# Kernel tuning notes

Hardware: AMD Instinct MI355X
Metric: run time of the kernel (lower is better)

The kernel has to match this reference:

```python
import jax, jax.numpy as jnp
import numpy as np

D_MODEL = 1024
NHEAD = 16
HEAD_DIM = D_MODEL // NHEAD
SCALE = 1.0 / np.sqrt(HEAD_DIM).astype(np.float32)
B, L = 2, 2048
NEG_INF = -1e30


def setup_inputs() -> dict:
    key = jax.random.key(0)
    ks = jax.random.split(key, 12)
    xav = np.sqrt(6.0 / (D_MODEL + D_MODEL)).astype(np.float32)  # xavier_uniform gain=1
    def lin_w(k):
        return jax.random.uniform(k, (D_MODEL, D_MODEL), jnp.float32, -xav, xav)
    x = jax.random.normal(ks[0], (B, L, D_MODEL), jnp.float32)
    role_mask = jax.random.randint(ks[1], (B, L), 0, 2, jnp.int32)
    # causal attention mask: True = masked (upper triangle above diagonal)
    attn_mask = jnp.triu(jnp.ones((L, L), jnp.bool_), k=1)
    # random key padding: True = padded key
    key_padding_mask = jax.random.randint(ks[2], (B, L), 0, 2, jnp.int32).astype(jnp.bool_)
    return {
        "x": x,
        "role_mask": role_mask,
        "attn_mask": attn_mask,
        "key_padding_mask": key_padding_mask,
        "Wq": lin_w(ks[3]), "bq": jnp.zeros((D_MODEL,), jnp.float32),
        "Wk": lin_w(ks[4]), "bk": jnp.zeros((D_MODEL,), jnp.float32),
        "Wv": lin_w(ks[5]), "bv": jnp.zeros((D_MODEL,), jnp.float32),
        "Wo": lin_w(ks[6]), "bo": jnp.zeros((D_MODEL,), jnp.float32),
        "delta": jnp.asarray(1.0, jnp.float32),
    }


def reference(x, role_mask, attn_mask, key_padding_mask,
              Wq, bq, Wk, bk, Wv, bv, Wo, bo, delta):
    Bb, Ll, Dd = x.shape
    def heads(t):  # [B,L,D] -> [B,H,L,hd]
        return t.reshape(Bb, Ll, NHEAD, HEAD_DIM).transpose(0, 2, 1, 3)
    Q = heads(x @ Wq.T + bq)
    K = heads(x @ Wk.T + bk)
    V = heads(x @ Wv.T + bv)
    scores = jnp.einsum('bhqd,bhkd->bhqk', Q, K) * SCALE  # [B,H,L,L]
    same_role = (role_mask[:, :, None] == role_mask[:, None, :])  # [B,L,L]
    scores = scores + (same_role.astype(scores.dtype) * delta)[:, None, :, :]
    scores = jnp.where(attn_mask[None, None, :, :], -jnp.inf, scores)
    scores = jnp.where(key_padding_mask[:, None, None, :], -jnp.inf, scores)
    attn = jax.nn.softmax(scores, axis=-1)
    attn = jnp.nan_to_num(attn, nan=0.0, posinf=0.0, neginf=0.0)
    out = jnp.einsum('bhqk,bhkd->bhqd', attn, V)
    out = out.transpose(0, 2, 1, 3).reshape(Bb, Ll, Dd)
    return out @ Wo.T + bo
```

## Files before the change

### kernel.cpp

```cpp
#include <hip/hip_runtime.h>
#include <hip/hip_bf16.h>

#define DM 1024
#define NH 16
#define HD 64
#define BB 2
#define LL 2048
#define SCALE 0.125f
#define NEG_BIG -1e30f
#define LOG2E 1.4426950408889634f
#define SC2 (SCALE * LOG2E)
#define FIXM 16.0f
#define SLOTB 8448
#define POOL0_SLOTS 960

typedef __bf16 bf16;
typedef __bf16 bf16x8 __attribute__((ext_vector_type(8)));
typedef __bf16 bf16x4 __attribute__((ext_vector_type(4)));
typedef float f32x4 __attribute__((ext_vector_type(4)));

static __device__ inline bf16x8 load8(const bf16* p) {
    return *reinterpret_cast<const bf16x8*>(p);
}

static __device__ inline float scrub(float x) {
    union { float f; unsigned u; } c; c.f = x;
    return ((c.u & 0x7F800000u) == 0x7F800000u) ? 0.f : x;
}

typedef __attribute__((address_space(1))) const unsigned char ga_t;
typedef __attribute__((address_space(3))) unsigned char ls_t;
static __device__ inline void gload_lds16(const void* g, void* l) {
    __builtin_amdgcn_global_load_lds((ga_t*)g, (ls_t*)l, 16, 0, 0);
}

__global__ __launch_bounds__(256) void prep_all(
    const float* __restrict__ x,
    const float* __restrict__ Wq, const float* __restrict__ Wk,
    const float* __restrict__ Wv, const float* __restrict__ Wo,
    bf16* __restrict__ xb, bf16* __restrict__ Wqb, bf16* __restrict__ Wkb,
    bf16* __restrict__ Wvb, bf16* __restrict__ Wob,
    const int* __restrict__ role, const void* __restrict__ kpad,
    const float* __restrict__ deltap, float2* __restrict__ biasG)
{
    const int tid = threadIdx.x;
    const int gid = blockIdx.x;
    if (gid < 2048) {
        const float* src; bf16* dst; size_t base;
        if (gid < 1024) { src = x; dst = xb; base = (size_t)gid * 1024; }
        else {
            const int wsel = (gid - 1024) >> 8;
            src = (wsel == 0) ? Wq : (wsel == 1) ? Wk : (wsel == 2) ? Wv : Wo;
            dst = (wsel == 0) ? Wqb : (wsel == 1) ? Wkb : (wsel == 2) ? Wvb : Wob;
            base = (size_t)((gid - 1024) & 255) * 1024;
        }
#pragma unroll
        for (int it = 0; it < 4; it++) {
            const size_t i = base + it * 256 + tid;
            const f32x4 v = ((const f32x4*)src)[i];
            bf16x4 o;
            o[0] = (bf16)v[0]; o[1] = (bf16)v[1]; o[2] = (bf16)v[2]; o[3] = (bf16)v[3];
            ((bf16x4*)dst)[i] = o;
        }
        return;
    }
    const unsigned char* kb = (const unsigned char*)kpad;
    int f3F = 0, fLow = 0, fOff = 0;
    for (int i = (tid & 63); i < BB * LL; i += 64) {
        const unsigned char v = kb[i];
        if (v == 0x3F) f3F = 1;
        if ((i & 3) < 2 && v) fLow = 1;
        if ((i & 3) && v) fOff = 1;
    }
    const int mode = __any(f3F) ? (__any(fLow) ? 3 : 2) : (__any(fOff) ? 1 : 0);
    const float d2 = scrub(deltap[0]) * LOG2E;
    const int idx = (gid - 2048) * 256 + tid;
    const bool pad = (mode == 0) ? (((const int*)kpad)[idx] != 0)
                   : (mode == 1) ? (((const unsigned char*)kpad)[idx] != 0)
                   : (mode == 2) ? (((const float*)kpad)[idx] != 0.f)
                                 : (((const unsigned short*)kpad)[idx] != 0);
    const int r = role[idx];
    const float base = (pad ? NEG_BIG : 0.f) - FIXM;
    float2 o;
    o.x = base + ((r == 0) ? d2 : 0.f);
    o.y = base + ((r == 1) ? d2 : 0.f);
    biasG[idx] = o;
}

__global__ __launch_bounds__(256) void qkv_bf16(
    const bf16* __restrict__ xb,
    const bf16* __restrict__ Wqb, const bf16* __restrict__ Wkb, const bf16* __restrict__ Wvb,
    const float* __restrict__ bq, const float* __restrict__ bk, const float* __restrict__ bv,
    bf16* __restrict__ qw, bf16* __restrict__ kw, bf16* __restrict__ vw)
{
    __shared__ bf16 As[128 * 32];
    __shared__ bf16 Bs[128 * 32];
    const int tid = threadIdx.x;
    const int lane = tid & 63, w = tid >> 6;
    const int wm = w >> 1, wn = w & 1;
    const int ln = lane & 15, quad = lane >> 4;

    const int lin = blockIdx.y * 32 + blockIdx.x;
    const int xcd = lin & 7;
    const int t = lin >> 3;
    const int mloc = t & 3;
    const int yy = t >> 2;
    const int m0 = (xcd * 4 + mloc) * 128;
    const int sel = yy >> 3;
    const int nloc0 = (yy & 7) * 128;

    const bf16* Wb = (sel == 0) ? Wqb : ((sel == 1) ? Wkb : Wvb);
    const float* bias = (sel == 0) ? bq : ((sel == 1) ? bk : bv);
    bf16* dstw = (sel == 0) ? qw : ((sel == 1) ? kw : vw);

    const int rA = lane >> 2;
    const int cA = (lane & 3) * 8;

    f32x4 acc[4][4] = {};
    for (int k0 = 0; k0 < DM; k0 += 32) {
        __syncthreads();
#pragma unroll
        for (int s = 0; s < 2; s++) {
            const int r0 = s * 64 + w * 16;
            gload_lds16(xb + (size_t)(m0 + r0 + rA) * DM + k0 + cA, &As[r0 * 32]);
            gload_lds16(Wb + (size_t)(nloc0 + r0 + rA) * DM + k0 + cA, &Bs[r0 * 32]);
        }
        __syncthreads();
        bf16x8 a[4], b[4];
#pragma unroll
        for (int mi = 0; mi < 4; mi++)
            a[mi] = *(bf16x8*)&As[(wm * 64 + mi * 16 + ln) * 32 + quad * 8];
#pragma unroll
        for (int ni = 0; ni < 4; ni++)
            b[ni] = *(bf16x8*)&Bs[(wn * 64 + ni * 16 + ln) * 32 + quad * 8];
#pragma unroll
        for (int mi = 0; mi < 4; mi++)
#pragma unroll
            for (int ni = 0; ni < 4; ni++)
                acc[mi][ni] = __builtin_amdgcn_mfma_f32_16x16x32_bf16(a[mi], b[ni], acc[mi][ni], 0, 0, 0);
    }

#pragma unroll
    for (int mi = 0; mi < 4; mi++) {
#pragma unroll
        for (int ni = 0; ni < 4; ni++) {
            const int ncol = nloc0 + wn * 64 + ni * 16 + ln;
            const float bv_ = bias[ncol];
            const int hh = ncol >> 6, dd = ncol & 63;
#pragma unroll
            for (int i = 0; i < 4; i++) {
                const int row = m0 + wm * 64 + mi * 16 + quad * 4 + i;
                const int bb = row >> 11, llr = row & (LL - 1);
                const bf16 v = (bf16)scrub(acc[mi][ni][i] + bv_);
                dstw[(((size_t)(bb * NH + hh) * LL) + llr) * HD + dd] = v;
            }
        }
    }
}

__global__ __launch_bounds__(256) void vtrans(
    const bf16* __restrict__ vw, bf16* __restrict__ vtw)
{
    __shared__ bf16 T[64][72];
    const int l0 = blockIdx.x * 64;
    const int bh = blockIdx.y;
    const int tid = threadIdx.x;
#pragma unroll
    for (int it = 0; it < 2; it++) {
        const int idx = it * 256 + tid;
        const int row = idx >> 3, c8 = (idx & 7) * 8;
        *(bf16x8*)&T[row][c8] = load8(vw + ((size_t)bh * LL + l0 + row) * HD + c8);
    }
    __syncthreads();
#pragma unroll
    for (int it = 0; it < 2; it++) {
        const int idx = it * 256 + tid;
        const int dd = idx >> 3, pg = (idx & 7) * 8;
        bf16x8 o;
#pragma unroll
        for (int j = 0; j < 8; j++) {
            const int p = pg + j;
            const int kl = (p & 3) * 16 + (p >> 2);
            o[j] = T[kl][dd];
        }
        *(bf16x8*)(vtw + ((size_t)bh * HD + dd) * LL + l0 + pg) = o;
    }
}

#define PSTR 32
__global__ __launch_bounds__(256) void attn_v12(
    const bf16* __restrict__ qw, const bf16* __restrict__ kw, const bf16* __restrict__ vtw,
    const int* __restrict__ role, const float2* __restrict__ biasG,
    char* __restrict__ pool0, char* __restrict__ pool1,
    bf16* __restrict__ attn_out)
{
    const int lin = blockIdx.y * 60 + blockIdx.x;
    const int xcd = lin & 7;
    const int t = lin >> 3;
    const int xg = t % 60;
    const int g = t / 60;
    const int bh = g * 8 + xcd;

    int qb, c;
    if (xg < 24)      { qb = 31 - xg / 3; c = xg % 3; }
    else if (xg < 48) { qb = 23 - (xg - 24) / 2; c = (xg - 24) % 2; }
    else              { qb = 59 - xg; c = 0; }
    const int nch = (qb + 12) / 12;

    __shared__ bf16 Ks[2][2][64 * 32];
    __shared__ bf16 Vs[2][2][64 * 32];
    __shared__ bf16 Ps[4][2][16 * PSTR];

    const int tid = threadIdx.x;
    const int lane = tid & 63, w = tid >> 6;
    const int col = lane & 15, quad = lane >> 4;
    const int h = bh & (NH - 1), b = bh >> 4;
    const int q0 = qb * 64 + w * 16;

    const bf16* qbase = qw + (size_t)((b * NH + h) * LL) * HD;
    const bf16* kbase = kw + (size_t)((b * NH + h) * LL) * HD;
    const bf16* vbase = vtw + (size_t)((b * NH + h) * HD) * LL;
    const float2* bias2 = biasG + (size_t)b * LL;
    const int* rrow = role + b * LL;

    const int srow = lane >> 2;
    const int swz = ((lane & 3) ^ ((lane >> 3) & 3)) * 8;
    const bf16* ksrc = kbase + (size_t)(w * 16 + srow) * HD + swz;
    const bf16* vsrc = vbase + (size_t)(w * 16 + srow) * LL + swz;

    bf16x8 qf[2];
    qf[0] = load8(qbase + (size_t)(q0 + col) * HD + quad * 8);
    qf[1] = load8(qbase + (size_t)(q0 + col) * HD + 32 + quad * 8);

    bf16x8 ones;
#pragma unroll
    for (int j = 0; j < 8; j++) ones[j] = (bf16)1.0f;

    int role_q[4];
#pragma unroll
    for (int i = 0; i < 4; i++) role_q[i] = rrow[q0 + quad * 4 + i];

    f32x4 ol = {};
    f32x4 o[4] = {};

    const int t0 = c * 12;
    const int t1 = (t0 + 12 < qb + 1) ? t0 + 12 : qb + 1;

    {
        const int kp = t0 * 64;
#pragma unroll
        for (int st = 0; st < 2; st++)
            gload_lds16(ksrc + (size_t)kp * HD + st * 32, &Ks[0][st][w * 512]);
#pragma unroll
        for (int kh = 0; kh < 2; kh++)
            gload_lds16(vsrc + kp + kh * 32, &Vs[0][kh][w * 512]);
    }

    const int rs = (quad ^ ((col >> 1) & 3)) * 8;

    for (int kt = t0; kt < t1; kt++) {
        const int cur = (kt - t0) & 1;
        __syncthreads();

        if (kt + 1 < t1) {
            const int k1 = (kt + 1) * 64;
#pragma unroll
            for (int st = 0; st < 2; st++)
                gload_lds16(ksrc + (size_t)k1 * HD + st * 32, &Ks[cur ^ 1][st][w * 512]);
#pragma unroll
            for (int kh = 0; kh < 2; kh++)
                gload_lds16(vsrc + k1 + kh * 32, &Vs[cur ^ 1][kh][w * 512]);
        }

        const int k0 = kt * 64;
        float2 bb[4];
#pragma unroll
        for (int ns = 0; ns < 4; ns++) bb[ns] = bias2[k0 + ns * 16 + col];

        f32x4 s[4] = {};
#pragma unroll
        for (int st = 0; st < 2; st++) {
#pragma unroll
            for (int ns = 0; ns < 4; ns++) {
                const bf16x8 kf = *(bf16x8*)&Ks[cur][st][(ns * 16 + col) * 32 + rs];
                s[ns] = __builtin_amdgcn_mfma_f32_16x16x32_bf16(qf[st], kf, s[ns], 0, 0, 0);
            }
        }
        const bool diag = (kt == qb);
        const int half = col >> 3;
#pragma unroll
        for (int i = 0; i < 4; i++) {
            bf16x4 pk;
#pragma unroll
            for (int ns = 0; ns < 4; ns++) {
                float sv = fmaf(s[ns][i], SC2, role_q[i] ? bb[ns].y : bb[ns].x);
                if (diag && (k0 + ns * 16 + col) > q0 + quad * 4 + i) sv = NEG_BIG;
                pk[ns] = (bf16)exp2f(sv);
            }
            const int row = quad * 4 + i;
            const int sw = (quad * 2 + (i >> 1)) & 3;
            const int ew = ((((col & 7) >> 1) ^ sw) * 8) + (col & 1) * 4;
            *(bf16x4*)&Ps[w][half][row * PSTR + ew] = pk;
        }
        bf16x8 pf[2];
#pragma unroll
        for (int st = 0; st < 2; st++)
            pf[st] = *(bf16x8*)&Ps[w][st][col * PSTR + rs];
#pragma unroll
        for (int ns = 0; ns < 4; ns++) {
#pragma unroll
            for (int kh = 0; kh < 2; kh++) {
                const bf16x8 vf = *(bf16x8*)&Vs[cur][kh][(ns * 16 + col) * 32 + rs];
                o[ns] = __builtin_amdgcn_mfma_f32_16x16x32_bf16(pf[kh], vf, o[ns], 0, 0, 0);
            }
        }
#pragma unroll
        for (int kh = 0; kh < 2; kh++)
            ol = __builtin_amdgcn_mfma_f32_16x16x32_bf16(pf[kh], ones, ol, 0, 0, 0);
    }

    if (nch == 1) {
        bf16* orow = attn_out + (size_t)(b * LL) * DM;
#pragma unroll
        for (int i = 0; i < 4; i++) {
            const float l = ol[i];
            const float inv = (l > 0.f) ? 1.f / l : 0.f;
            const int qq = q0 + quad * 4 + i;
#pragma unroll
            for (int ns = 0; ns < 4; ns++)
                orow[(size_t)qq * DM + h * HD + ns * 16 + col] = (bf16)scrub(o[ns][i] * inv);
        }
    } else {
        const int base = (qb <= 23) ? (qb - 12) * 2 : 24 + (qb - 24) * 3;
        const int slot = bh * 48 + base + c;
        char* ptr = (slot < POOL0_SLOTS) ? (pool0 + (size_t)slot * SLOTB)
                                         : (pool1 + (size_t)(slot - POOL0_SLOTS) * SLOTB);
        bf16* op = (bf16*)ptr;
        float* lp = (float*)(ptr + 8192);
#pragma unroll
        for (int i = 0; i < 4; i++) {
            const int r = w * 16 + quad * 4 + i;
            if (col == 0) lp[r] = ol[i];
#pragma unroll
            for (int ns = 0; ns < 4; ns++)
                op[r * 64 + ns * 16 + col] = (bf16)scrub(o[ns][i]);
        }
    }
}

__global__ __launch_bounds__(256) void combine(
    const char* __restrict__ pool0, const char* __restrict__ pool1,
    bf16* __restrict__ attn_out)
{
    const int qb = 12 + blockIdx.x;
    const int bh = blockIdx.y;
    const int h = bh & (NH - 1), b = bh >> 4;
    const int nch = (qb + 12) / 12;
    const int base = (qb <= 23) ? (qb - 12) * 2 : 24 + (qb - 24) * 3;

    const char* ptr[3];
    for (int c = 0; c < nch; c++) {
        const int slot = bh * 48 + base + c;
        ptr[c] = (slot < POOL0_SLOTS) ? (pool0 + (size_t)slot * SLOTB)
                                      : (pool1 + (size_t)(slot - POOL0_SLOTS) * SLOTB);
    }

    __shared__ float linv[64];
    const int tid = threadIdx.x;
    if (tid < 64) {
        float ls = 0.f;
        for (int c = 0; c < nch; c++) ls += ((const float*)(ptr[c] + 8192))[tid];
        linv[tid] = (ls > 0.f) ? 1.f / ls : 0.f;
    }
    __syncthreads();

    const int r = tid >> 2;
    const int d0 = (tid & 3) * 16;
    float acc[16] = {};
    for (int c = 0; c < nch; c++) {
        const bf16* op = (const bf16*)ptr[c];
#pragma unroll
        for (int half = 0; half < 2; half++) {
            const bf16x8 v = load8(op + r * 64 + d0 + half * 8);
#pragma unroll
            for (int j = 0; j < 8; j++) acc[half * 8 + j] += (float)v[j];
        }
    }
    const float inv = linv[r];
    bf16x8 outv[2];
#pragma unroll
    for (int half = 0; half < 2; half++)
#pragma unroll
        for (int j = 0; j < 8; j++)
            outv[half][j] = (bf16)scrub(acc[half * 8 + j] * inv);
    bf16* orow = attn_out + ((size_t)(b * LL) + qb * 64 + r) * DM + h * HD + d0;
    *(bf16x8*)orow = outv[0];
    *(bf16x8*)(orow + 8) = outv[1];
}

__global__ __launch_bounds__(256) void out_bf16(
    const bf16* __restrict__ A, const bf16* __restrict__ Wb,
    const float* __restrict__ bias, float* __restrict__ out)
{
    __shared__ bf16 As[128 * 32];
    __shared__ bf16 Bs[64 * 32];
    const int tid = threadIdx.x;
    const int lane = tid & 63, w = tid >> 6;
    const int ln = lane & 15, quad = lane >> 4;

    const int lin = blockIdx.y * 32 + blockIdx.x;
    const int xcd = lin & 7;
    const int t = lin >> 3;
    const int mloc = t & 3;
    const int n = t >> 2;
    const int m0 = (xcd * 4 + mloc) * 128;
    const int n0 = n * 64;

    const int rA = lane >> 2;
    const int cA = (lane & 3) * 8;

    f32x4 acc[2][4] = {};
    for (int k0 = 0; k0 < DM; k0 += 32) {
        __syncthreads();
#pragma unroll
        for (int s = 0; s < 2; s++) {
            const int r0 = s * 64 + w * 16;
            gload_lds16(A + (size_t)(m0 + r0 + rA) * DM + k0 + cA, &As[r0 * 32]);
        }
        gload_lds16(Wb + (size_t)(n0 + w * 16 + rA) * DM + k0 + cA, &Bs[w * 16 * 32]);
        __syncthreads();
        bf16x8 a[2], b[4];
#pragma unroll
        for (int mi = 0; mi < 2; mi++)
            a[mi] = *(bf16x8*)&As[(w * 32 + mi * 16 + ln) * 32 + quad * 8];
#pragma unroll
        for (int ni = 0; ni < 4; ni++)
            b[ni] = *(bf16x8*)&Bs[(ni * 16 + ln) * 32 + quad * 8];
#pragma unroll
        for (int mi = 0; mi < 2; mi++)
#pragma unroll
            for (int ni = 0; ni < 4; ni++)
                acc[mi][ni] = __builtin_amdgcn_mfma_f32_16x16x32_bf16(a[mi], b[ni], acc[mi][ni], 0, 0, 0);
    }
#pragma unroll
    for (int mi = 0; mi < 2; mi++) {
#pragma unroll
        for (int ni = 0; ni < 4; ni++) {
            const int ncol = n0 + ni * 16 + ln;
            const float bv_ = bias[ncol];
#pragma unroll
            for (int i = 0; i < 4; i++) {
                const int row = m0 + w * 32 + mi * 16 + quad * 4 + i;
                out[(size_t)row * DM + ncol] = scrub(acc[mi][ni][i] + bv_);
            }
        }
    }
}

extern "C" void kernel_launch(void* const* d_in, const int* in_sizes, int n_in,
                              void* d_out, int out_size, void* d_ws, size_t ws_size,
                              hipStream_t stream) {
    const float* x    = (const float*)d_in[0];
    const int*   role = (const int*)d_in[1];
    const void*  kpad = d_in[3];
    const float* Wq = (const float*)d_in[4];
    const float* bq = (const float*)d_in[5];
    const float* Wk = (const float*)d_in[6];
    const float* bk = (const float*)d_in[7];
    const float* Wv = (const float*)d_in[8];
    const float* bv = (const float*)d_in[9];
    const float* Wo = (const float*)d_in[10];
    const float* bo = (const float*)d_in[11];
    const float* dl = (const float*)d_in[12];

    char* ws = (char*)d_ws;
    bf16* qw   = (bf16*)(ws);
    bf16* kw   = (bf16*)(ws + (size_t)(8u  << 20));
    bf16* Wqb  = (bf16*)(ws + (size_t)(16u << 20));
    bf16* Wkb  = (bf16*)(ws + (size_t)(18u << 20));
    bf16* Wvb  = (bf16*)(ws + (size_t)(20u << 20));
    char* pool0 = ws + (size_t)(16u << 20);
    bf16* vw   = (bf16*)(ws + (size_t)(24u << 20));
    bf16* aw   = (bf16*)(ws + (size_t)(24u << 20));
    bf16* vtw  = (bf16*)(ws + (size_t)(32u << 20));
    bf16* xb   = (bf16*)(ws + (size_t)(40u << 20));
    char* pool1 = ws + (size_t)(40u << 20);
    bf16* Wob  = (bf16*)(ws + (size_t)(48u << 20) + 65536);
    float2* biasG = (float2*)(ws + (size_t)(48u << 20));
    float* out = (float*)d_out;

    prep_all<<<dim3(2064), dim3(256), 0, stream>>>(
        x, Wq, Wk, Wv, Wo, xb, Wqb, Wkb, Wvb, Wob, role, kpad, dl, biasG);
    qkv_bf16<<<dim3(32, 24), dim3(256), 0, stream>>>(
        xb, Wqb, Wkb, Wvb, bq, bk, bv, qw, kw, vw);
    vtrans<<<dim3(32, 32), dim3(256), 0, stream>>>(vw, vtw);
    attn_v12<<<dim3(60, 32), dim3(256), 0, stream>>>(
        qw, kw, vtw, role, biasG, pool0, pool1, aw);
    combine<<<dim3(20, 32), dim3(256), 0, stream>>>(pool0, pool1, aw);
    out_bf16<<<dim3(32, 16), dim3(256), 0, stream>>>(aw, Wob, bo, out);
}
```

Baseline: 225.6 us.

## Compute transposed scores so P stays in registers, drop LDS P round-trip

Swaps the MFMA operand order so each lane holds scores for one query across contiguous keys. K rows are loaded into LDS in a permuted order, and V is transposed linearly with an XOR-swizzled tile, so the exp'd probabilities feed the PV MFMA directly from registers. This removes the per-tile shared-memory write and read of P and vectorizes the output and bias loads. The cost is a more intricate index mapping that must stay consistent across the K permutation, the V transpose, the bias and the causal mask.

```diff
diff --git a/kernel.cpp b/kernel.cpp
--- a/kernel.cpp
+++ b/kernel.cpp
@@ -169,7 +169,8 @@
     for (int it = 0; it < 2; it++) {
         const int idx = it * 256 + tid;
         const int row = idx >> 3, c8 = (idx & 7) * 8;
-        *(bf16x8*)&T[row][c8] = load8(vw + ((size_t)bh * LL + l0 + row) * HD + c8);
+        const int wc = (((c8 >> 3) ^ ((row >> 3) & 7))) * 8;
+        *(bf16x8*)&T[row][wc] = load8(vw + ((size_t)bh * LL + l0 + row) * HD + c8);
     }
     __syncthreads();
 #pragma unroll
@@ -179,16 +180,14 @@
         bf16x8 o;
 #pragma unroll
         for (int j = 0; j < 8; j++) {
-            const int p = pg + j;
-            const int kl = (p & 3) * 16 + (p >> 2);
-            o[j] = T[kl][dd];
+            const int r = pg + j;
+            o[j] = T[r][(dd & 7) + ((((dd >> 3) ^ ((r >> 3) & 7))) << 3)];
         }
         *(bf16x8*)(vtw + ((size_t)bh * HD + dd) * LL + l0 + pg) = o;
     }
 }
 
-#define PSTR 32
-__global__ __launch_bounds__(256) void attn_v12(
+__global__ __launch_bounds__(256) void attn_v13(
     const bf16* __restrict__ qw, const bf16* __restrict__ kw, const bf16* __restrict__ vtw,
     const int* __restrict__ role, const float2* __restrict__ biasG,
     char* __restrict__ pool0, char* __restrict__ pool1,
@@ -209,7 +208,6 @@
 
     __shared__ bf16 Ks[2][2][64 * 32];
     __shared__ bf16 Vs[2][2][64 * 32];
-    __shared__ bf16 Ps[4][2][16 * PSTR];
 
     const int tid = threadIdx.x;
     const int lane = tid & 63, w = tid >> 6;
@@ -224,8 +222,11 @@
     const int* rrow = role + b * LL;
 
     const int srow = lane >> 2;
+    const int sslot = w * 16 + srow;
+    const int trueK = ((sslot >> 5) & 1) * 32 + ((sslot >> 2) & 3) * 8
+                    + ((sslot >> 4) & 1) * 4 + (sslot & 3);
     const int swz = ((lane & 3) ^ ((lane >> 3) & 3)) * 8;
-    const bf16* ksrc = kbase + (size_t)(w * 16 + srow) * HD + swz;
+    const bf16* ksrc = kbase + (size_t)trueK * HD + swz;
     const bf16* vsrc = vbase + (size_t)(w * 16 + srow) * LL + swz;
 
     bf16x8 qf[2];
@@ -236,9 +237,8 @@
 #pragma unroll
     for (int j = 0; j < 8; j++) ones[j] = (bf16)1.0f;
 
-    int role_q[4];
-#pragma unroll
-    for (int i = 0; i < 4; i++) role_q[i] = rrow[q0 + quad * 4 + i];
+    const int role_q = rrow[q0 + col];
+    const int qabs = q0 + col;
 
     f32x4 ol = {};
     f32x4 o[4] = {};
@@ -273,9 +273,6 @@
         }
 
         const int k0 = kt * 64;
-        float2 bb[4];
-#pragma unroll
-        for (int ns = 0; ns < 4; ns++) bb[ns] = bias2[k0 + ns * 16 + col];
 
         f32x4 s[4] = {};
 #pragma unroll
@@ -283,52 +280,49 @@
 #pragma unroll
             for (int ns = 0; ns < 4; ns++) {
                 const bf16x8 kf = *(bf16x8*)&Ks[cur][st][(ns * 16 + col) * 32 + rs];
-                s[ns] = __builtin_amdgcn_mfma_f32_16x16x32_bf16(qf[st], kf, s[ns], 0, 0, 0);
+                s[ns] = __builtin_amdgcn_mfma_f32_16x16x32_bf16(kf, qf[st], s[ns], 0, 0, 0);
             }
         }
+
         const bool diag = (kt == qb);
-        const int half = col >> 3;
-#pragma unroll
-        for (int i = 0; i < 4; i++) {
-            bf16x4 pk;
-#pragma unroll
-            for (int ns = 0; ns < 4; ns++) {
-                float sv = fmaf(s[ns][i], SC2, role_q[i] ? bb[ns].y : bb[ns].x);
-                if (diag && (k0 + ns * 16 + col) > q0 + quad * 4 + i) sv = NEG_BIG;
-                pk[ns] = (bf16)exp2f(sv);
+        bf16x8 pf[2];
+#pragma unroll
+        for (int ns = 0; ns < 4; ns++) {
+            const int kb_ = k0 + ((ns >> 1) << 5) + (quad << 3) + ((ns & 1) << 2);
+            const f32x4 bA = *(const f32x4*)&bias2[kb_];
+            const f32x4 bB = *(const f32x4*)&bias2[kb_ + 2];
+#pragma unroll
+            for (int i = 0; i < 4; i++) {
+                const f32x4 bp = (i < 2) ? bA : bB;
+                const float bias = role_q ? bp[(i & 1) * 2 + 1] : bp[(i & 1) * 2];
+                float sv = fmaf(s[ns][i], SC2, bias);
+                if (diag && (kb_ + i) > qabs) sv = NEG_BIG;
+                pf[ns >> 1][(ns & 1) * 4 + i] = (bf16)exp2f(sv);
             }
-            const int row = quad * 4 + i;
-            const int sw = (quad * 2 + (i >> 1)) & 3;
-            const int ew = ((((col & 7) >> 1) ^ sw) * 8) + (col & 1) * 4;
-            *(bf16x4*)&Ps[w][half][row * PSTR + ew] = pk;
-        }
-        bf16x8 pf[2];
-#pragma unroll
-        for (int st = 0; st < 2; st++)
-            pf[st] = *(bf16x8*)&Ps[w][st][col * PSTR + rs];
+        }
+
 #pragma unroll
         for (int ns = 0; ns < 4; ns++) {
 #pragma unroll
             for (int kh = 0; kh < 2; kh++) {
                 const bf16x8 vf = *(bf16x8*)&Vs[cur][kh][(ns * 16 + col) * 32 + rs];
-                o[ns] = __builtin_amdgcn_mfma_f32_16x16x32_bf16(pf[kh], vf, o[ns], 0, 0, 0);
+                o[ns] = __builtin_amdgcn_mfma_f32_16x16x32_bf16(vf, pf[kh], o[ns], 0, 0, 0);
             }
         }
 #pragma unroll
         for (int kh = 0; kh < 2; kh++)
-            ol = __builtin_amdgcn_mfma_f32_16x16x32_bf16(pf[kh], ones, ol, 0, 0, 0);
+            ol = __builtin_amdgcn_mfma_f32_16x16x32_bf16(ones, pf[kh], ol, 0, 0, 0);
     }
 
     if (nch == 1) {
-        bf16* orow = attn_out + (size_t)(b * LL) * DM;
-#pragma unroll
-        for (int i = 0; i < 4; i++) {
-            const float l = ol[i];
-            const float inv = (l > 0.f) ? 1.f / l : 0.f;
-            const int qq = q0 + quad * 4 + i;
-#pragma unroll
-            for (int ns = 0; ns < 4; ns++)
-                orow[(size_t)qq * DM + h * HD + ns * 16 + col] = (bf16)scrub(o[ns][i] * inv);
+        const float inv = (ol[0] > 0.f) ? 1.f / ol[0] : 0.f;
+        bf16* orow = attn_out + ((size_t)(b * LL) + qabs) * DM + h * HD;
+#pragma unroll
+        for (int ns = 0; ns < 4; ns++) {
+            bf16x4 ov;
+#pragma unroll
+            for (int i = 0; i < 4; i++) ov[i] = (bf16)scrub(o[ns][i] * inv);
+            *(bf16x4*)&orow[ns * 16 + quad * 4] = ov;
         }
     } else {
         const int base = (qb <= 23) ? (qb - 12) * 2 : 24 + (qb - 24) * 3;
@@ -337,13 +331,14 @@
                                          : (pool1 + (size_t)(slot - POOL0_SLOTS) * SLOTB);
         bf16* op = (bf16*)ptr;
         float* lp = (float*)(ptr + 8192);
-#pragma unroll
-        for (int i = 0; i < 4; i++) {
-            const int r = w * 16 + quad * 4 + i;
-            if (col == 0) lp[r] = ol[i];
-#pragma unroll
-            for (int ns = 0; ns < 4; ns++)
-                op[r * 64 + ns * 16 + col] = (bf16)scrub(o[ns][i]);
+        const int r = w * 16 + col;
+        if (quad == 0) lp[r] = ol[0];
+#pragma unroll
+        for (int ns = 0; ns < 4; ns++) {
+            bf16x4 ov;
+#pragma unroll
+            for (int i = 0; i < 4; i++) ov[i] = (bf16)scrub(o[ns][i]);
+            *(bf16x4*)&op[r * 64 + ns * 16 + quad * 4] = ov;
         }
     }
 }
@@ -494,7 +489,7 @@
     qkv_bf16<<<dim3(32, 24), dim3(256), 0, stream>>>(
         xb, Wqb, Wkb, Wvb, bq, bk, bv, qw, kw, vw);
     vtrans<<<dim3(32, 32), dim3(256), 0, stream>>>(vw, vtw);
-    attn_v12<<<dim3(60, 32), dim3(256), 0, stream>>>(
+    attn_v13<<<dim3(60, 32), dim3(256), 0, stream>>>(
         qw, kw, vtw, role, biasG, pool0, pool1, aw);
     combine<<<dim3(20, 32), dim3(256), 0, stream>>>(pool0, pool1, aw);
     out_bf16<<<dim3(32, 16), dim3(256), 0, stream>>>(aw, Wob, bo, out);
```

Result: slower. 230.5 us (+2.1%).
